# Performance work log

Hardware: AMD Instinct MI355X
Metric: run time of the kernel (lower is better)

## Reference

```python
import jax, jax.numpy as jnp
import numpy as np

N_HEADS = 16
E = 1024
HEAD = E // N_HEADS

def setup_inputs() -> dict:
    key = jax.random.key(0)
    k1, k2, k3, k4 = jax.random.split(key, 4)
    x = jax.random.normal(k1, (4, 2048, E), dtype=jnp.float32)
    # Linear weights stored as (in, out) for x @ W
    W_kqv = jax.random.normal(k2, (E, 3 * E), dtype=jnp.float32) * (E ** -0.5)
    W_proj = jax.random.normal(k3, (E, E), dtype=jnp.float32) * (E ** -0.5)
    b_proj = jax.random.normal(k4, (E,), dtype=jnp.float32) * 0.02
    return {"x": x, "W_kqv": W_kqv, "W_proj": W_proj, "b_proj": b_proj}

def reference(x, W_kqv, W_proj, b_proj):
    B, T, Edim = x.shape
    kqv = x @ W_kqv  # [B,T,3E]
    k, q, v = jnp.split(kqv, 3, axis=-1)
    # [B,T,E] -> [B,H,T,D]
    def to_heads(t):
        return t.reshape(B, T, N_HEADS, HEAD).transpose(0, 2, 1, 3)
    k, q, v = to_heads(k), to_heads(q), to_heads(v)
    att = jnp.einsum('bhqd,bhkd->bhqk', q, k) * (HEAD ** -0.5)
    causal = jnp.tril(jnp.ones((T, T), dtype=bool))
    att = jnp.where(causal[None, None], att, jnp.float32(-jnp.inf))
    att = jax.nn.softmax(att, axis=-1)  # dropout p=0 (eval)
    x_att = jnp.einsum('bhqk,bhkd->bhqd', att, v)
    x_att = x_att.transpose(0, 2, 1, 3).reshape(B, T, Edim)
    return x_att @ W_proj + b_proj
```

## Files before the change

### kernel.cpp

```cpp
#include <hip/hip_runtime.h>
#include <hip/hip_bf16.h>


typedef __bf16 bf16_t;
typedef __bf16 bf16x8 __attribute__((ext_vector_type(8)));
typedef __bf16 bf16x4 __attribute__((ext_vector_type(4)));
typedef float  f32x4  __attribute__((ext_vector_type(4)));

#define GLD16(gp, lp) __builtin_amdgcn_global_load_lds(                        \
    (const __attribute__((address_space(1))) void*)(gp),                       \
    (__attribute__((address_space(3))) void*)(lp), 16, 0, 0)

static constexpr int kB = 4, kT = 2048, kE = 1024, kH = 16, kD = 64;
static constexpr int kM = kB * kT;
static constexpr int kN1 = 3 * kE;
static constexpr float kScale = 0.125f;
static constexpr float kShift = 10.0f;

__global__ void cvt_f32_bf16(const float* __restrict__ in,
                             bf16_t* __restrict__ out, int n4) {
  int i = blockIdx.x * 256 + threadIdx.x;
  if (i >= n4) return;
  float4 f = reinterpret_cast<const float4*>(in)[i];
  bf16x4 o = { (bf16_t)f.x, (bf16_t)f.y, (bf16_t)f.z, (bf16_t)f.w };
  reinterpret_cast<bf16x4*>(out)[i] = o;
}

__global__ void transpose_tile(const float* __restrict__ W,
                               bf16_t* __restrict__ Wt, int K, int N) {
  __shared__ bf16_t t[64][65];
  const int k0 = blockIdx.x * 64, n0 = blockIdx.y * 64;
  const int c = threadIdx.x & 63, r4 = threadIdx.x >> 6;
#pragma unroll
  for (int i = 0; i < 16; i++) {
    const int kk = r4 * 16 + i;
    t[kk][c] = (bf16_t)W[(size_t)(k0 + kk) * N + n0 + c];
  }
  __syncthreads();
#pragma unroll
  for (int i = 0; i < 16; i++) {
    const int nn = r4 * 16 + i;
    Wt[(size_t)(n0 + nn) * K + k0 + c] = t[c][nn];
  }
}

template <int MODE>
__global__ __launch_bounds__(256, 2)
void gemm_bt(const bf16_t* __restrict__ A, const bf16_t* __restrict__ Bt,
             float* __restrict__ Cout, const float* __restrict__ bias,
             bf16_t* __restrict__ Kh, bf16_t* __restrict__ Qh,
             bf16_t* __restrict__ Vt, int M, int N, int K) {
  constexpr int BM = 128, BN = 128, BK = 64;
  __shared__ __align__(16) bf16_t As[BM * BK];
  __shared__ __align__(16) bf16_t Bs[BN * BK];
  const int tid = threadIdx.x;
  const int lane = tid & 63, wave = tid >> 6;
  const int m0 = blockIdx.y * BM, n0 = blockIdx.x * BN;
  const int wr = (wave >> 1) * 64, wc = (wave & 1) * 64;
  const int l15 = lane & 15, l4 = lane >> 4;
  const int r8 = lane >> 3, c8 = lane & 7;

  f32x4 acc[4][4];
#pragma unroll
  for (int m = 0; m < 4; m++)
#pragma unroll
    for (int n = 0; n < 4; n++) acc[m][n] = f32x4{0.f, 0.f, 0.f, 0.f};

  for (int k0 = 0; k0 < K; k0 += BK) {
    const bf16_t* Ag = A + (size_t)(m0 + wave * 32) * K + k0;
    const bf16_t* Bg = Bt + (size_t)(n0 + wave * 32) * K + k0;
    bf16_t* Al = As + wave * 32 * BK;
    bf16_t* Bl = Bs + wave * 32 * BK;
#pragma unroll
    for (int i = 0; i < 4; i++) {
      GLD16(Ag + (size_t)(i * 8 + r8) * K + c8 * 8, Al + i * 8 * BK);
      GLD16(Bg + (size_t)(i * 8 + r8) * K + c8 * 8, Bl + i * 8 * BK);
    }
    __syncthreads();
#pragma unroll
    for (int ks = 0; ks < 2; ks++) {
      bf16x8 af[4], bfr[4];
#pragma unroll
      for (int m = 0; m < 4; m++)
        af[m] = *reinterpret_cast<const bf16x8*>(
            As + (wr + m * 16 + l15) * BK + ks * 32 + l4 * 8);
#pragma unroll
      for (int n = 0; n < 4; n++)
        bfr[n] = *reinterpret_cast<const bf16x8*>(
            Bs + (wc + n * 16 + l15) * BK + ks * 32 + l4 * 8);
#pragma unroll
      for (int m = 0; m < 4; m++)
#pragma unroll
        for (int n = 0; n < 4; n++)
          acc[m][n] = __builtin_amdgcn_mfma_f32_16x16x32_bf16(
              af[m], bfr[n], acc[m][n], 0, 0, 0);
    }
    __syncthreads();
  }

#pragma unroll
  for (int m = 0; m < 4; m++) {
#pragma unroll
    for (int n = 0; n < 4; n++) {
      const int gcol = n0 + wc + n * 16 + l15;
      const int growb = m0 + wr + m * 16 + l4 * 4;
      if constexpr (MODE == 0) {
        const int seg = gcol >> 10, idx = gcol & 1023;
        const int h = idx >> 6, d = idx & 63;
        const int b = growb >> 11, t = growb & 2047;
        if (seg == 2) {
          bf16x4 pv = { (bf16_t)acc[m][n][0], (bf16_t)acc[m][n][1],
                        (bf16_t)acc[m][n][2], (bf16_t)acc[m][n][3] };
          *reinterpret_cast<bf16x4*>(
              Vt + ((size_t)(b * 16 + h) * 64 + d) * 2048 + t) = pv;
        } else {
          bf16_t* tgt = (seg == 0) ? Kh : Qh;
          const float sc = (seg == 1) ? kScale : 1.0f;
#pragma unroll
          for (int j = 0; j < 4; j++)
            tgt[((size_t)(b * 16 + h) * 2048 + (t + j)) * 64 + d] =
                (bf16_t)(acc[m][n][j] * sc);
        }
      } else {
        const float bv = bias[gcol];
#pragma unroll
        for (int j = 0; j < 4; j++)
          Cout[(size_t)(growb + j) * N + gcol] = acc[m][n][j] + bv;
      }
    }
  }
}

__global__ __launch_bounds__(256, 3)
void attn_fwd(const bf16_t* __restrict__ Qh, const bf16_t* __restrict__ Kh,
              const bf16_t* __restrict__ Vt, bf16_t* __restrict__ xatt) {
  const int bx = blockIdx.x;
  const int qt = 15 - (bx >> 6);
  const int bh = bx & 63;
  const int b = bh >> 4, h = bh & 15;
  const bf16_t* Qp = Qh + (size_t)bh * kT * kD;
  const bf16_t* Kp = Kh + (size_t)bh * kT * kD;
  const bf16_t* Vp = Vt + (size_t)bh * kD * kT;
  __shared__ __align__(16) bf16_t Ks[2][64 * 64];
  __shared__ __align__(16) bf16_t Vs[2][64 * 64];
  __shared__ __align__(16) bf16_t Ps[128 * 64];
  const int tid = threadIdx.x, lane = tid & 63, wave = tid >> 6;
  const int l15 = lane & 15, l4 = lane >> 4;
  const int r8 = lane >> 3, c8 = lane & 7;
  const int qr = wave * 32;
  const int swc = (c8 ^ r8) * 8;
  const int swr = (l15 & 7) * 8;
  const int q0 = qt * 128;
  const int nkt = qt * 2 + 2;

  auto stage = [&](int buf, int kt) {
    const int k0 = kt * 64;
#pragma unroll
    for (int i = 0; i < 2; i++) {
      const int row = wave * 16 + i * 8 + r8;
      GLD16(Kp + (size_t)(k0 + row) * kD + swc,
            Ks[buf] + (wave * 16 + i * 8) * 64);
      GLD16(Vp + (size_t)row * kT + k0 + swc,
            Vs[buf] + (wave * 16 + i * 8) * 64);
    }
  };

  bf16x8 qf[2][2];
#pragma unroll
  for (int m = 0; m < 2; m++)
#pragma unroll
    for (int ks = 0; ks < 2; ks++)
      qf[m][ks] = *reinterpret_cast<const bf16x8*>(
          Qp + (size_t)(q0 + qr + m * 16 + l15) * kD + ks * 32 + l4 * 8);

  bf16x8 ones;
#pragma unroll
  for (int e = 0; e < 8; e++) ones[e] = (bf16_t)1.0f;

  f32x4 oacc[2][4];
  f32x4 lacc[2];
#pragma unroll
  for (int m = 0; m < 2; m++) {
    lacc[m] = f32x4{0.f, 0.f, 0.f, 0.f};
#pragma unroll
    for (int dn = 0; dn < 4; dn++) oacc[m][dn] = f32x4{0.f, 0.f, 0.f, 0.f};
  }

  stage(0, 0);
  __syncthreads();
  int cur = 0;
  for (int kt = 0; kt < nkt; kt++) {
    const int k0 = kt * 64;
    if (kt + 1 < nkt) stage(cur ^ 1, kt + 1);

    const bool active = (k0 <= q0 + qr + 31);
    if (active) {
      f32x4 s[2][4];
#pragma unroll
      for (int m = 0; m < 2; m++)
#pragma unroll
        for (int n = 0; n < 4; n++) s[m][n] = f32x4{0.f, 0.f, 0.f, 0.f};
      __builtin_amdgcn_s_setprio(1);
#pragma unroll
      for (int ks = 0; ks < 2; ks++) {
        bf16x8 kf[4];
#pragma unroll
        for (int n = 0; n < 4; n++)
          kf[n] = *reinterpret_cast<const bf16x8*>(
              Ks[cur] + (n * 16 + l15) * 64 + (((ks * 4 + l4) * 8) ^ swr));
#pragma unroll
        for (int m = 0; m < 2; m++)
#pragma unroll
          for (int n = 0; n < 4; n++)
            s[m][n] = __builtin_amdgcn_mfma_f32_16x16x32_bf16(
                qf[m][ks], kf[n], s[m][n], 0, 0, 0);
      }
      __builtin_amdgcn_s_setprio(0);

      if (k0 + 63 > q0 + qr) {
#pragma unroll
        for (int m = 0; m < 2; m++)
#pragma unroll
          for (int n = 0; n < 4; n++)
#pragma unroll
            for (int j = 0; j < 4; j++) {
              const int qg = q0 + qr + m * 16 + l4 * 4 + j;
              const int kg = k0 + n * 16 + l15;
              if (kg > qg) s[m][n][j] = -__builtin_inff();
            }
      }

#pragma unroll
      for (int m = 0; m < 2; m++)
#pragma unroll
        for (int n = 0; n < 4; n++)
#pragma unroll
          for (int j = 0; j < 4; j++) {
            const int pr = qr + m * 16 + l4 * 4 + j;
            Ps[pr * 64 + ((n * 16 + l15) ^ ((pr & 7) << 3))] =
                (bf16_t)__expf(s[m][n][j] - kShift);
          }

      __builtin_amdgcn_s_setprio(1);
#pragma unroll
      for (int ks = 0; ks < 2; ks++) {
        bf16x8 pf[2], vf[4];
#pragma unroll
        for (int m = 0; m < 2; m++)
          pf[m] = *reinterpret_cast<const bf16x8*>(
              Ps + (qr + m * 16 + l15) * 64 + (((ks * 4 + l4) * 8) ^ swr));
#pragma unroll
        for (int dn = 0; dn < 4; dn++)
          vf[dn] = *reinterpret_cast<const bf16x8*>(
              Vs[cur] + (dn * 16 + l15) * 64 + (((ks * 4 + l4) * 8) ^ swr));
#pragma unroll
        for (int m = 0; m < 2; m++) {
#pragma unroll
          for (int dn = 0; dn < 4; dn++)
            oacc[m][dn] = __builtin_amdgcn_mfma_f32_16x16x32_bf16(
                pf[m], vf[dn], oacc[m][dn], 0, 0, 0);
          lacc[m] = __builtin_amdgcn_mfma_f32_16x16x32_bf16(
              pf[m], ones, lacc[m], 0, 0, 0);
        }
      }
      __builtin_amdgcn_s_setprio(0);
    }
    __syncthreads();
    cur ^= 1;
  }

#pragma unroll
  for (int m = 0; m < 2; m++) {
    float inv[4];
#pragma unroll
    for (int j = 0; j < 4; j++) inv[j] = 1.f / lacc[m][j];
#pragma unroll
    for (int dn = 0; dn < 4; dn++)
#pragma unroll
      for (int j = 0; j < 4; j++) {
        const int t = q0 + qr + m * 16 + l4 * 4 + j;
        const int col = h * 64 + dn * 16 + l15;
        xatt[((size_t)b * kT + t) * kE + col] =
            (bf16_t)(oacc[m][dn][j] * inv[j]);
      }
  }
}

extern "C" void kernel_launch(void* const* d_in, const int* in_sizes, int n_in,
                              void* d_out, int out_size, void* d_ws,
                              size_t ws_size, hipStream_t stream) {
  const float* x     = (const float*)d_in[0];
  const float* Wkqv  = (const float*)d_in[1];
  const float* Wproj = (const float*)d_in[2];
  const float* bproj = (const float*)d_in[3];
  float* out = (float*)d_out;

  char* ws = (char*)d_ws;
  bf16_t* xb     = (bf16_t*)(ws);
  bf16_t* WkqvT  = (bf16_t*)(ws + 16777216);
  bf16_t* WprojT = (bf16_t*)(ws + 23068672);
  bf16_t* Qh     = (bf16_t*)(ws + 25165824);
  bf16_t* Kh     = (bf16_t*)(ws + 41943040);
  bf16_t* Vt     = (bf16_t*)(ws + 58720256);
  bf16_t* xatt   = (bf16_t*)(ws + 75497472);

  cvt_f32_bf16<<<(kM * kE / 4 + 255) / 256, 256, 0, stream>>>(x, xb, kM * kE / 4);
  transpose_tile<<<dim3(kE / 64, kN1 / 64), 256, 0, stream>>>(Wkqv, WkqvT, kE, kN1);
  transpose_tile<<<dim3(kE / 64, kE / 64), 256, 0, stream>>>(Wproj, WprojT, kE, kE);

  gemm_bt<0><<<dim3(kN1 / 128, kM / 128), 256, 0, stream>>>(
      xb, WkqvT, nullptr, nullptr, Kh, Qh, Vt, kM, kN1, kE);

  attn_fwd<<<dim3(16 * 64), 256, 0, stream>>>(Qh, Kh, Vt, xatt);

  gemm_bt<1><<<dim3(kE / 128, kM / 128), 256, 0, stream>>>(
      xatt, WprojT, out, bproj, nullptr, nullptr, nullptr, kM, kE, kE);
}
```

Measured before the change: 171.3 us.

## Double-buffer GEMM with MFMA-ordered LDS staging and enlarge attention blocks to 512 threads

The GEMM now double-buffers its K tiles in two half-phases. Loads are issued one tile ahead with explicit vmcnt waits and raw barriers, which replaces the two __syncthreads per iteration, and MFMA issue priority is raised. Data is staged into LDS already in MFMA fragment order, so each lane reads its fragment contiguously. The attention kernel now uses 8 waves covering 256 query rows per block, which halves the grid and shares each K/V tile across more rows. The risks are reduced occupancy from doubled LDS and a larger Ps buffer, and more load imbalance between causal tiles.

```diff
diff --git a/kernel.cpp b/kernel.cpp
--- a/kernel.cpp
+++ b/kernel.cpp
@@ -10,6 +10,8 @@
 #define GLD16(gp, lp) __builtin_amdgcn_global_load_lds(                        \
     (const __attribute__((address_space(1))) void*)(gp),                       \
     (__attribute__((address_space(3))) void*)(lp), 16, 0, 0)
+
+#define WAITV(n) asm volatile("s_waitcnt vmcnt(" #n ")" ::: "memory")
 
 static constexpr int kB = 4, kT = 2048, kE = 1024, kH = 16, kD = 64;
 static constexpr int kM = kB * kT;
@@ -46,19 +48,31 @@
 
 template <int MODE>
 __global__ __launch_bounds__(256, 2)
-void gemm_bt(const bf16_t* __restrict__ A, const bf16_t* __restrict__ Bt,
-             float* __restrict__ Cout, const float* __restrict__ bias,
-             bf16_t* __restrict__ Kh, bf16_t* __restrict__ Qh,
-             bf16_t* __restrict__ Vt, int M, int N, int K) {
-  constexpr int BM = 128, BN = 128, BK = 64;
-  __shared__ __align__(16) bf16_t As[BM * BK];
-  __shared__ __align__(16) bf16_t Bs[BN * BK];
-  const int tid = threadIdx.x;
-  const int lane = tid & 63, wave = tid >> 6;
-  const int m0 = blockIdx.y * BM, n0 = blockIdx.x * BN;
-  const int wr = (wave >> 1) * 64, wc = (wave & 1) * 64;
+void gemm_2ph(const bf16_t* __restrict__ A, const bf16_t* __restrict__ Bt,
+              float* __restrict__ Cout, const float* __restrict__ bias,
+              bf16_t* __restrict__ Kh, bf16_t* __restrict__ Qh,
+              bf16_t* __restrict__ Vt, int M, int N, int K) {
+  __shared__ __align__(16) bf16_t As_[2][2][4096];
+  __shared__ __align__(16) bf16_t Bs_[2][2][4096];
+  const int tid = threadIdx.x, lane = tid & 63, wave = tid >> 6;
   const int l15 = lane & 15, l4 = lane >> 4;
-  const int r8 = lane >> 3, c8 = lane & 7;
+  const int m0 = blockIdx.y * 128, n0 = blockIdx.x * 128;
+  const int NT = K >> 6;
+  const bf16_t* Ag = A + (size_t)m0 * K;
+  const bf16_t* Bg = Bt + (size_t)n0 * K;
+  const int wrh = wave >> 1, wch = wave & 1;
+
+  auto HS = [&](int t, int h, int bi) {
+    const int k0 = t << 6;
+#pragma unroll
+    for (int i = 0; i < 2; i++) {
+      const size_t roff =
+          (size_t)((i * 4 + wave) * 16 + l15) * K + k0 + h * 32 + l4 * 8;
+      const int ds = (i * 256 + wave * 64) * 8;
+      GLD16(Ag + roff, &As_[bi][h][ds]);
+      GLD16(Bg + roff, &Bs_[bi][h][ds]);
+    }
+  };
 
   f32x4 acc[4][4];
 #pragma unroll
@@ -66,38 +80,44 @@
 #pragma unroll
     for (int n = 0; n < 4; n++) acc[m][n] = f32x4{0.f, 0.f, 0.f, 0.f};
 
-  for (int k0 = 0; k0 < K; k0 += BK) {
-    const bf16_t* Ag = A + (size_t)(m0 + wave * 32) * K + k0;
-    const bf16_t* Bg = Bt + (size_t)(n0 + wave * 32) * K + k0;
-    bf16_t* Al = As + wave * 32 * BK;
-    bf16_t* Bl = Bs + wave * 32 * BK;
-#pragma unroll
-    for (int i = 0; i < 4; i++) {
-      GLD16(Ag + (size_t)(i * 8 + r8) * K + c8 * 8, Al + i * 8 * BK);
-      GLD16(Bg + (size_t)(i * 8 + r8) * K + c8 * 8, Bl + i * 8 * BK);
-    }
-    __syncthreads();
-#pragma unroll
-    for (int ks = 0; ks < 2; ks++) {
+  HS(0, 0, 0);
+  HS(0, 1, 0);
+
+#pragma unroll 1
+  for (int t = 0; t < NT; t++) {
+    const int bi = t & 1;
+#pragma unroll
+    for (int h = 0; h < 2; h++) {
+      if (t + 1 < NT) {
+        HS(t + 1, h, bi ^ 1);
+        WAITV(8);
+      } else if (h == 0) {
+        WAITV(4);
+      } else {
+        WAITV(0);
+      }
+      __builtin_amdgcn_s_barrier();
       bf16x8 af[4], bfr[4];
 #pragma unroll
-      for (int m = 0; m < 4; m++)
-        af[m] = *reinterpret_cast<const bf16x8*>(
-            As + (wr + m * 16 + l15) * BK + ks * 32 + l4 * 8);
-#pragma unroll
-      for (int n = 0; n < 4; n++)
-        bfr[n] = *reinterpret_cast<const bf16x8*>(
-            Bs + (wc + n * 16 + l15) * BK + ks * 32 + l4 * 8);
+      for (int r = 0; r < 4; r++)
+        af[r] = *reinterpret_cast<const bf16x8*>(
+            &As_[bi][h][((wrh * 4 + r) * 64 + lane) * 8]);
+#pragma unroll
+      for (int c = 0; c < 4; c++)
+        bfr[c] = *reinterpret_cast<const bf16x8*>(
+            &Bs_[bi][h][((wch * 4 + c) * 64 + lane) * 8]);
+      __builtin_amdgcn_s_setprio(1);
 #pragma unroll
       for (int m = 0; m < 4; m++)
 #pragma unroll
         for (int n = 0; n < 4; n++)
           acc[m][n] = __builtin_amdgcn_mfma_f32_16x16x32_bf16(
               af[m], bfr[n], acc[m][n], 0, 0, 0);
+      __builtin_amdgcn_s_setprio(0);
     }
-    __syncthreads();
-  }
-
+  }
+
+  const int wr = wrh * 64, wc = wch * 64;
 #pragma unroll
   for (int m = 0; m < 4; m++) {
 #pragma unroll
@@ -131,11 +151,11 @@
   }
 }
 
-__global__ __launch_bounds__(256, 3)
+__global__ __launch_bounds__(512, 4)
 void attn_fwd(const bf16_t* __restrict__ Qh, const bf16_t* __restrict__ Kh,
               const bf16_t* __restrict__ Vt, bf16_t* __restrict__ xatt) {
   const int bx = blockIdx.x;
-  const int qt = 15 - (bx >> 6);
+  const int qt = 7 - (bx >> 6);
   const int bh = bx & 63;
   const int b = bh >> 4, h = bh & 15;
   const bf16_t* Qp = Qh + (size_t)bh * kT * kD;
@@ -143,26 +163,21 @@
   const bf16_t* Vp = Vt + (size_t)bh * kD * kT;
   __shared__ __align__(16) bf16_t Ks[2][64 * 64];
   __shared__ __align__(16) bf16_t Vs[2][64 * 64];
-  __shared__ __align__(16) bf16_t Ps[128 * 64];
+  __shared__ __align__(16) bf16_t Ps[256 * 64];
   const int tid = threadIdx.x, lane = tid & 63, wave = tid >> 6;
   const int l15 = lane & 15, l4 = lane >> 4;
   const int r8 = lane >> 3, c8 = lane & 7;
   const int qr = wave * 32;
   const int swc = (c8 ^ r8) * 8;
   const int swr = (l15 & 7) * 8;
-  const int q0 = qt * 128;
-  const int nkt = qt * 2 + 2;
+  const int q0 = qt * 256;
+  const int nkt = qt * 4 + 4;
 
   auto stage = [&](int buf, int kt) {
     const int k0 = kt * 64;
-#pragma unroll
-    for (int i = 0; i < 2; i++) {
-      const int row = wave * 16 + i * 8 + r8;
-      GLD16(Kp + (size_t)(k0 + row) * kD + swc,
-            Ks[buf] + (wave * 16 + i * 8) * 64);
-      GLD16(Vp + (size_t)row * kT + k0 + swc,
-            Vs[buf] + (wave * 16 + i * 8) * 64);
-    }
+    const int row = wave * 8 + r8;
+    GLD16(Kp + (size_t)(k0 + row) * kD + swc, Ks[buf] + (wave * 8) * 64);
+    GLD16(Vp + (size_t)row * kT + k0 + swc, Vs[buf] + (wave * 8) * 64);
   };
 
   bf16x8 qf[2][2];
@@ -308,11 +323,11 @@
   transpose_tile<<<dim3(kE / 64, kN1 / 64), 256, 0, stream>>>(Wkqv, WkqvT, kE, kN1);
   transpose_tile<<<dim3(kE / 64, kE / 64), 256, 0, stream>>>(Wproj, WprojT, kE, kE);
 
-  gemm_bt<0><<<dim3(kN1 / 128, kM / 128), 256, 0, stream>>>(
+  gemm_2ph<0><<<dim3(kN1 / 128, kM / 128), 256, 0, stream>>>(
       xb, WkqvT, nullptr, nullptr, Kh, Qh, Vt, kM, kN1, kE);
 
-  attn_fwd<<<dim3(16 * 64), 256, 0, stream>>>(Qh, Kh, Vt, xatt);
-
-  gemm_bt<1><<<dim3(kE / 128, kM / 128), 256, 0, stream>>>(
+  attn_fwd<<<dim3(8 * 64), 512, 0, stream>>>(Qh, Kh, Vt, xatt);
+
+  gemm_2ph<1><<<dim3(kE / 128, kM / 128), 256, 0, stream>>>(
       xatt, WprojT, out, bproj, nullptr, nullptr, nullptr, kM, kE, kE);
 }
```

Measured after the change: 323.6 us. 88.9% more time.
